# Kernel optimization log

Measured on AMD Instinct MI355X. Metric: run time of the kernel, lower is better.

Reference implementation:

```python
import jax, jax.numpy as jnp
import numpy as np

ALPHA = 0.1

def ewma(y, alpha=ALPHA):
    # y: [B, T, D]; x_ewma[0] = y[0], x_ewma[t] = alpha*y[t] + (1-alpha)*x_ewma[t-1]
    y_t = jnp.swapaxes(y, 0, 1)  # [T, B, D]
    def step(carry, xt):
        c = alpha * xt + (1.0 - alpha) * carry
        return c, c
    _, out = jax.lax.scan(step, y_t[0], y_t[1:])  # [T-1, B, D]
    out = jnp.concatenate([y_t[:1], out], axis=0)  # [T, B, D]
    return jnp.swapaxes(out, 0, 1)


def setup_inputs() -> dict:
    key = jax.random.key(0)
    k1, k2, k3, k4, k5 = jax.random.split(key, 5)
    B, C, T, D = 32, 32, 2048, 512
    x = jax.random.normal(k1, (B, C, T), dtype=jnp.float32)
    W_ve = jax.random.normal(k2, (D, C), dtype=jnp.float32) * (1.0 / np.sqrt(C))
    b_ve = jax.random.normal(k3, (D,), dtype=jnp.float32) * 0.01
    W_lin = jax.random.normal(k4, (D, D), dtype=jnp.float32) * (1.0 / np.sqrt(D))
    b_lin = jax.random.normal(k5, (D,), dtype=jnp.float32) * 0.01
    return {"x": x, "W_ve": W_ve, "b_ve": b_ve, "W_lin": W_lin, "b_lin": b_lin}


def reference(x, W_ve, b_ve, W_lin, b_lin):
    # x: [B, C, T] -> [B, T, C]
    xt = jnp.transpose(x, (0, 2, 1))
    B, T, C = xt.shape
    # first-difference with leading zero row
    x_diff = jnp.concatenate(
        [jnp.zeros((B, 1, C), dtype=xt.dtype), xt[:, 1:, :] - xt[:, :-1, :]], axis=1
    )
    # value embedding: Linear(C -> D)
    x_emb = jnp.einsum("btc,dc->btd", x_diff, W_ve) + b_ve
    # bidirectional EWMA smoothing
    x_lr = ewma(x_emb)
    x_rl = jnp.flip(ewma(jnp.flip(x_emb, axis=1)), axis=1)
    x_smooth = (x_lr + x_rl) * 0.5
    # output projection: Linear(D -> D)
    return jnp.einsum("btd,ed->bte", x_smooth, W_lin) + b_lin
```

## Files before the change

kernel.cpp:

```cpp
#include <hip/hip_runtime.h>

constexpr int B = 32, C = 32, T = 2048, D = 512;
constexpr float ALPHA = 0.1f;
constexpr float BETA  = 0.9f;
constexpr float LOG2_BETA = -0.15200309344504997f;
constexpr float BETA16    = 0.18530201888518410f;
constexpr float BETA14    = 0.22876792454961000f;

typedef float floatx4 __attribute__((ext_vector_type(4)));

constexpr int CHUNK = 128;
constexpr int SUB   = 16;
constexpr int SUBH  = 14;
constexpr int NSUB  = CHUNK / SUB;
constexpr int HALO  = NSUB * SUBH;
constexpr int LEAD  = 116;
constexpr int WIN   = LEAD + CHUNK + HALO;
constexpr int PAD   = WIN + 1;

__global__ __launch_bounds__(256) void combine_weights(
    const float* __restrict__ W_ve, const float* __restrict__ b_ve,
    const float* __restrict__ W_lin, const float* __restrict__ b_lin,
    float* __restrict__ W_comb, float* __restrict__ b_comb) {
  int e  = blockIdx.x;
  int c  = threadIdx.x & 31;
  int ds = threadIdx.x >> 5;
  float acc = 0.f, accb = 0.f;
#pragma unroll 4
  for (int i = 0; i < 64; ++i) {
    int d = ds * 64 + i;
    float wl = W_lin[e * D + d];
    acc  += wl * W_ve[d * C + c];
    accb += wl * b_ve[d];
  }
  __shared__ float red[8][33];
  __shared__ float redb[8];
  red[ds][c] = acc;
  if (c == 0) redb[ds] = accb;
  __syncthreads();
  if (ds == 0) {
    float ssum = 0.f;
#pragma unroll
    for (int k = 0; k < 8; ++k) ssum += red[k][c];
    W_comb[e * C + c] = ssum;
    if (c == 0) {
      float sb = 0.f;
#pragma unroll
      for (int k = 0; k < 8; ++k) sb += redb[k];
      b_comb[e] = sb + b_lin[e];
    }
  }
}

__global__ __launch_bounds__(256, 3) void fused_main(
    const float* __restrict__ x, const float* __restrict__ W_comb,
    const float* __restrict__ b_comb, float* __restrict__ out) {
  int b   = blockIdx.y;
  int t0  = blockIdx.x * CHUNK;
  int wlo = t0 - LEAD;

  __shared__ float xl[C * PAD];
  __shared__ float Lf[2][NSUB][C];
  __shared__ float Lb[2][NSUB][C];
  const float* xb = x + (size_t)b * C * T;

  int c   = threadIdx.x & 31;
  int sub = threadIdx.x >> 5;

  float dlast = xb[c * T + (T - 1)] - xb[c * T + (T - 2)];

  if (wlo >= 0 && wlo + WIN <= T) {
    for (int idx = threadIdx.x; idx < C * (WIN / 4); idx += 256) {
      int cc = idx / (WIN / 4);
      int q  = idx - cc * (WIN / 4);
      float4 v   = *(const float4*)(xb + cc * T + wlo + 4 * q);
      float* dst = xl + cc * PAD + 4 * q;
      dst[0] = v.x; dst[1] = v.y; dst[2] = v.z; dst[3] = v.w;
    }
  } else {
    for (int idx = threadIdx.x; idx < C * WIN; idx += 256) {
      int cc = idx / WIN;
      int tt = idx - cc * WIN;
      int t  = min(max(wlo + tt, 0), T - 1);
      xl[cc * PAD + tt] = xb[cc * T + t];
    }
  }
  __syncthreads();

  int ts = t0 + sub * SUB;
  const float* xc = xl + c * PAD - wlo;
#define DD(t) (xc[(t)] - xc[(t) - 1])

  int ha = t0 - HALO  + sub * SUBH;
  int ba = t0 + CHUNK + sub * SUBH;
  float fh = 0.f, bh = 0.f;
#pragma unroll
  for (int i = 0; i < SUBH; ++i) {
    fh = ALPHA * DD(ha + i)            + BETA * fh;
    bh = ALPHA * DD(ba + SUBH - 1 - i) + BETA * bh;
  }
  float lr[SUB], rl[SUB];
  float fm = 0.f, bm = 0.f;
#pragma unroll
  for (int i = 0; i < SUB; ++i) {
    fm = ALPHA * DD(ts + i) + BETA * fm;
    lr[i] = fm;
    bm = ALPHA * DD(ts + SUB - 1 - i) + BETA * bm;
    rl[SUB - 1 - i] = bm;
  }
  Lf[0][sub][c] = fh;
  Lf[1][sub][c] = lr[SUB - 1];
  Lb[0][sub][c] = bh;
  Lb[1][sub][c] = rl[0];
  __syncthreads();
#undef DD

  float Cc = 0.f, Bc = 0.f;
#pragma unroll
  for (int h = 0; h < NSUB; ++h) {
    Cc = BETA14 * Cc + Lf[0][h][c];
    Bc = BETA14 * Bc + Lb[0][NSUB - 1 - h][c];
  }
#pragma unroll
  for (int j = 0; j < NSUB - 1; ++j) {
    float cn = BETA16 * Cc + Lf[1][j][c];
    float bn = BETA16 * Bc + Lb[1][NSUB - 1 - j][c];
    Cc = (j < sub)            ? cn : Cc;
    Bc = (NSUB - 1 - j > sub) ? bn : Bc;
  }
  float f = BETA * Cc;
#pragma unroll
  for (int i = 0; i < SUB; ++i) { lr[i] += f; f *= BETA; }
  float g = BETA * Bc;
  float e = exp2f((float)(T - ts - (SUB - 1)) * LOG2_BETA);
#pragma unroll
  for (int i = SUB - 1; i >= 0; --i) {
    lr[i] = 0.5f * (lr[i] + (rl[i] + g) + e * dlast);
    g *= BETA;
    e *= BETA;
  }

  float* sbuf = xl;
  {
    int tbase = sub * SUB;
#pragma unroll
    for (int i = 0; i < SUB; ++i) sbuf[(tbase + i) * C + c] = lr[i];
  }

  int li   = threadIdx.x & 127;
  int half = threadIdx.x >> 7;
  int e0   = li * 4;
  float w[4][C], bias[4];
#pragma unroll
  for (int j = 0; j < 4; ++j) {
    const float4* wr = (const float4*)(W_comb + (e0 + j) * C);
#pragma unroll
    for (int c4 = 0; c4 < C / 4; ++c4) {
      float4 wv = wr[c4];
      w[j][c4 * 4 + 0] = wv.x;
      w[j][c4 * 4 + 1] = wv.y;
      w[j][c4 * 4 + 2] = wv.z;
      w[j][c4 * 4 + 3] = wv.w;
    }
    bias[j] = b_comb[e0 + j];
  }
  __syncthreads();

  const float* srow = sbuf + half * (CHUNK / 2) * C;
  float* orow = out + ((size_t)b * T + t0 + half * (CHUNK / 2)) * D + e0;

#pragma unroll 2
  for (int t = 0; t < CHUNK / 2; ++t) {
    float a[4], a2[4];
#pragma unroll
    for (int j = 0; j < 4; ++j) { a[j] = bias[j]; a2[j] = 0.f; }
    const float4* sr4 = (const float4*)(srow + t * C);
#pragma unroll
    for (int c4 = 0; c4 < C / 4; ++c4) {
      float4 sv = sr4[c4];
      int cc = c4 * 4;
#pragma unroll
      for (int j = 0; j < 4; ++j) {
        a[j]  += sv.x * w[j][cc + 0];
        a2[j] += sv.y * w[j][cc + 1];
        a[j]  += sv.z * w[j][cc + 2];
        a2[j] += sv.w * w[j][cc + 3];
      }
    }
    floatx4 o;
    o.x = a[0] + a2[0];
    o.y = a[1] + a2[1];
    o.z = a[2] + a2[2];
    o.w = a[3] + a2[3];
    __builtin_nontemporal_store(o, (floatx4*)(orow + (size_t)t * D));
  }
}

extern "C" void kernel_launch(void* const* d_in, const int* in_sizes, int n_in,
                              void* d_out, int out_size, void* d_ws, size_t ws_size,
                              hipStream_t stream) {
  const float* x     = (const float*)d_in[0];
  const float* W_ve  = (const float*)d_in[1];
  const float* b_ve  = (const float*)d_in[2];
  const float* W_lin = (const float*)d_in[3];
  const float* b_lin = (const float*)d_in[4];
  float* out = (float*)d_out;

  float* W_comb = (float*)d_ws;
  float* b_comb = W_comb + (size_t)D * C;

  combine_weights<<<D, 256, 0, stream>>>(W_ve, b_ve, W_lin, b_lin, W_comb, b_comb);
  fused_main<<<dim3(T / CHUNK, B), 256, 0, stream>>>(x, W_comb, b_comb, out);
}
```

Before: 179.9 us.

## Compute output projection with split-bf16 MFMA instead of scalar FP32 FMAs

Replaces the scalar FP32 projection (32-wide K, 512 outputs) with bf16 MFMA 16x16x32 instructions. Each operand is split into hi and lo bf16 parts and three MFMAs are summed to keep near-FP32 accuracy. The combined weights are stored as pre-split bf16 pairs and the smoothed activations are split into LDS. The launch-bounds occupancy hint drops from 3 to 2. This trades VALU FMA work for matrix-core throughput, at the cost of some precision and more complex output store patterns.

```diff
diff --git a/kernel.cpp b/kernel.cpp
--- a/kernel.cpp
+++ b/kernel.cpp
@@ -7,7 +7,8 @@
 constexpr float BETA16    = 0.18530201888518410f;
 constexpr float BETA14    = 0.22876792454961000f;
 
-typedef float floatx4 __attribute__((ext_vector_type(4)));
+using short8 = __attribute__((ext_vector_type(8))) short;
+using f32x4  = __attribute__((ext_vector_type(4))) float;
 
 constexpr int CHUNK = 128;
 constexpr int SUB   = 16;
@@ -18,10 +19,22 @@
 constexpr int WIN   = LEAD + CHUNK + HALO;
 constexpr int PAD   = WIN + 1;
 
+__device__ __forceinline__ unsigned short rne_bf16(float f) {
+  unsigned int u = __float_as_uint(f);
+  return (unsigned short)((u + 0x7fffu + ((u >> 16) & 1u)) >> 16);
+}
+__device__ __forceinline__ void bf16_split(float v, unsigned short& hi,
+                                           unsigned short& lo) {
+  hi = rne_bf16(v);
+  float fh = __uint_as_float(((unsigned int)hi) << 16);
+  lo = rne_bf16(v - fh);
+}
+
 __global__ __launch_bounds__(256) void combine_weights(
     const float* __restrict__ W_ve, const float* __restrict__ b_ve,
     const float* __restrict__ W_lin, const float* __restrict__ b_lin,
-    float* __restrict__ W_comb, float* __restrict__ b_comb) {
+    unsigned short* __restrict__ w_hi, unsigned short* __restrict__ w_lo,
+    float* __restrict__ b_comb) {
   int e  = blockIdx.x;
   int c  = threadIdx.x & 31;
   int ds = threadIdx.x >> 5;
@@ -42,7 +55,10 @@
     float ssum = 0.f;
 #pragma unroll
     for (int k = 0; k < 8; ++k) ssum += red[k][c];
-    W_comb[e * C + c] = ssum;
+    unsigned short h, l;
+    bf16_split(ssum, h, l);
+    w_hi[e * C + c] = h;
+    w_lo[e * C + c] = l;
     if (c == 0) {
       float sb = 0.f;
 #pragma unroll
@@ -52,9 +68,10 @@
   }
 }
 
-__global__ __launch_bounds__(256, 3) void fused_main(
-    const float* __restrict__ x, const float* __restrict__ W_comb,
-    const float* __restrict__ b_comb, float* __restrict__ out) {
+__global__ __launch_bounds__(256, 2) void fused_main(
+    const float* __restrict__ x, const unsigned short* __restrict__ w_hi,
+    const unsigned short* __restrict__ w_lo, const float* __restrict__ b_comb,
+    float* __restrict__ out) {
   int b   = blockIdx.y;
   int t0  = blockIdx.x * CHUNK;
   int wlo = t0 - LEAD;
@@ -140,59 +157,52 @@
     e *= BETA;
   }
 
-  float* sbuf = xl;
+  unsigned short* sh = (unsigned short*)xl;
+  unsigned short* sl = sh + CHUNK * C;
   {
     int tbase = sub * SUB;
 #pragma unroll
-    for (int i = 0; i < SUB; ++i) sbuf[(tbase + i) * C + c] = lr[i];
-  }
-
-  int li   = threadIdx.x & 127;
-  int half = threadIdx.x >> 7;
-  int e0   = li * 4;
-  float w[4][C], bias[4];
-#pragma unroll
-  for (int j = 0; j < 4; ++j) {
-    const float4* wr = (const float4*)(W_comb + (e0 + j) * C);
-#pragma unroll
-    for (int c4 = 0; c4 < C / 4; ++c4) {
-      float4 wv = wr[c4];
-      w[j][c4 * 4 + 0] = wv.x;
-      w[j][c4 * 4 + 1] = wv.y;
-      w[j][c4 * 4 + 2] = wv.z;
-      w[j][c4 * 4 + 3] = wv.w;
-    }
-    bias[j] = b_comb[e0 + j];
-  }
-  __syncthreads();
-
-  const float* srow = sbuf + half * (CHUNK / 2) * C;
-  float* orow = out + ((size_t)b * T + t0 + half * (CHUNK / 2)) * D + e0;
-
+    for (int i = 0; i < SUB; ++i) {
+      unsigned short h, l;
+      bf16_split(lr[i], h, l);
+      sh[(tbase + i) * C + c] = h;
+      sl[(tbase + i) * C + c] = l;
+    }
+  }
+
+  int lane = threadIdx.x & 63;
+  int wid  = threadIdx.x >> 6;
+  int we0  = wid * 128;
+  int g8   = (lane >> 4) * 8;
+  int ecol = lane & 15;
+  short8 bwh[8], bwl[8];
+  float bias8[8];
+#pragma unroll
+  for (int et = 0; et < 8; ++et) {
+    int erow = we0 + et * 16 + ecol;
+    bwh[et] = *(const short8*)(w_hi + erow * C + g8);
+    bwl[et] = *(const short8*)(w_lo + erow * C + g8);
+    bias8[et] = b_comb[erow];
+  }
+  __syncthreads();
+
+  int a_off = ecol * C + g8;
 #pragma unroll 2
-  for (int t = 0; t < CHUNK / 2; ++t) {
-    float a[4], a2[4];
-#pragma unroll
-    for (int j = 0; j < 4; ++j) { a[j] = bias[j]; a2[j] = 0.f; }
-    const float4* sr4 = (const float4*)(srow + t * C);
-#pragma unroll
-    for (int c4 = 0; c4 < C / 4; ++c4) {
-      float4 sv = sr4[c4];
-      int cc = c4 * 4;
-#pragma unroll
-      for (int j = 0; j < 4; ++j) {
-        a[j]  += sv.x * w[j][cc + 0];
-        a2[j] += sv.y * w[j][cc + 1];
-        a[j]  += sv.z * w[j][cc + 2];
-        a2[j] += sv.w * w[j][cc + 3];
-      }
-    }
-    floatx4 o;
-    o.x = a[0] + a2[0];
-    o.y = a[1] + a2[1];
-    o.z = a[2] + a2[2];
-    o.w = a[3] + a2[3];
-    __builtin_nontemporal_store(o, (floatx4*)(orow + (size_t)t * D));
+  for (int tt = 0; tt < CHUNK / 16; ++tt) {
+    short8 a_hi = *(const short8*)(sh + tt * 16 * C + a_off);
+    short8 a_lo = *(const short8*)(sl + tt * 16 * C + a_off);
+    float* ob = out + ((size_t)b * T + t0 + tt * 16 + (lane >> 4) * 4) * D
+                + we0 + ecol;
+#pragma unroll
+    for (int et = 0; et < 8; ++et) {
+      f32x4 acc = {bias8[et], bias8[et], bias8[et], bias8[et]};
+      acc = __builtin_amdgcn_mfma_f32_16x16x32_bf16(a_hi, bwh[et], acc, 0, 0, 0);
+      acc = __builtin_amdgcn_mfma_f32_16x16x32_bf16(a_lo, bwh[et], acc, 0, 0, 0);
+      acc = __builtin_amdgcn_mfma_f32_16x16x32_bf16(a_hi, bwl[et], acc, 0, 0, 0);
+#pragma unroll
+      for (int r = 0; r < 4; ++r)
+        __builtin_nontemporal_store(acc[r], ob + (size_t)r * D + et * 16);
+    }
   }
 }
 
@@ -206,9 +216,10 @@
   const float* b_lin = (const float*)d_in[4];
   float* out = (float*)d_out;
 
-  float* W_comb = (float*)d_ws;
-  float* b_comb = W_comb + (size_t)D * C;
-
-  combine_weights<<<D, 256, 0, stream>>>(W_ve, b_ve, W_lin, b_lin, W_comb, b_comb);
-  fused_main<<<dim3(T / CHUNK, B), 256, 0, stream>>>(x, W_comb, b_comb, out);
-}
+  unsigned short* w_hi = (unsigned short*)d_ws;
+  unsigned short* w_lo = w_hi + (size_t)D * C;
+  float* b_comb        = (float*)(w_lo + (size_t)D * C);
+
+  combine_weights<<<D, 256, 0, stream>>>(W_ve, b_ve, W_lin, b_lin, w_hi, w_lo, b_comb);
+  fused_main<<<dim3(T / CHUNK, B), 256, 0, stream>>>(x, w_hi, w_lo, b_comb, out);
+}
```

Result: slower. 185.9 us (+3.3%).
